# Kernel optimization log

Measured on AMD Instinct MI355X. Metric: run time of the kernel, lower is better.

The kernel has to match this reference:

```python
import jax, jax.numpy as jnp
import numpy as np

DIM = 1024
C = 128
B = 8
T = 2048


def setup_inputs() -> dict:
    key = jax.random.key(0)
    ks = jax.random.split(key, 16)
    s = 0.02
    inp = {
        "x": jax.random.normal(ks[0], (B, T, DIM), dtype=jnp.float32),
        "Wq": jax.random.normal(ks[1], (DIM, C), dtype=jnp.float32) * s,
        "bq": jnp.zeros((C,), dtype=jnp.float32),
        "Wk": jax.random.normal(ks[2], (DIM, C), dtype=jnp.float32) * s,
        "bk": jnp.zeros((C,), dtype=jnp.float32),
        "Wv": jax.random.normal(ks[3], (DIM, C), dtype=jnp.float32) * s,
        "bv": jnp.zeros((C,), dtype=jnp.float32),
        "Wa": jax.random.normal(ks[4], (DIM, 1), dtype=jnp.float32) * s,
        "ba": jnp.zeros((1,), dtype=jnp.float32),
        "Wb": jax.random.normal(ks[5], (DIM, 1), dtype=jnp.float32) * s,
        "bb": jnp.zeros((1,), dtype=jnp.float32),
        "Wg": jax.random.normal(ks[6], (DIM, C), dtype=jnp.float32) * s,
        "bg": jnp.zeros((C,), dtype=jnp.float32),
        "Wo": jax.random.normal(ks[7], (C, DIM), dtype=jnp.float32) * s,
        "bo": jnp.zeros((DIM,), dtype=jnp.float32),
    }
    return inp


def reference(x, Wq, bq, Wk, bk, Wv, bv, Wa, ba, Wb, bb, Wg, bg, Wo, bo):
    # projections
    q = x @ Wq + bq                                   # [B,T,C]
    kr = x @ Wk + bk
    k = kr / jnp.maximum(jnp.linalg.norm(kr, axis=-1, keepdims=True), 1e-12)  # F.normalize
    v = x @ Wv + bv
    alpha = jax.nn.sigmoid(x @ Wa + ba)               # [B,T,1]
    beta = jax.nn.sigmoid(x @ Wb + bb)                # [B,T,1]
    gate = jax.nn.sigmoid(x @ Wg + bg)                # [B,T,C]

    def step(S, inp):
        q_t, k_t, v_t, a_t, b_t, g_t = inp            # [B,C],[B,C],[B,C],[B,1],[B,1],[B,C]
        # S @ (a*(I - b k k^T)) = a*(S - b*(S k) k^T)  (rank-1 form, no CxC bmm)
        Sk = jnp.einsum('bij,bj->bi', S, k_t)         # [B,C]
        a = a_t[:, :, None]                            # [B,1,1]
        b = b_t[:, :, None]
        S_new = a * (S - b * (Sk[:, :, None] * k_t[:, None, :])) \
                + b * (v_t[:, :, None] * k_t[:, None, :])
        o = jnp.einsum('bi,bij->bj', q_t, S_new) * g_t  # [B,C]
        return S_new, o

    seq = (
        jnp.swapaxes(q, 0, 1), jnp.swapaxes(k, 0, 1), jnp.swapaxes(v, 0, 1),
        jnp.swapaxes(alpha, 0, 1), jnp.swapaxes(beta, 0, 1), jnp.swapaxes(gate, 0, 1),
    )
    S0 = jnp.zeros((x.shape[0], C, C), dtype=x.dtype)
    _, outs = jax.lax.scan(step, S0, seq)             # [T,B,C]
    o = jnp.swapaxes(outs, 0, 1)                      # [B,T,C]
    return o @ Wo + bo                                # [B,T,DIM]
```

## Files before the change

kernel.cpp:

```cpp
#include <hip/hip_runtime.h>
#include <hip/hip_fp16.h>
#include <cstdint>

#define MB 8
#define TT 2048
#define DIMK 1024
#define CC 128
#define NG 32
#define MROWS (MB*TT)
#define NPROJ 576
#define YSTR 576

using bf16x8 = __attribute__((__ext_vector_type__(8))) __bf16;
using f32x4v = __attribute__((__ext_vector_type__(4))) float;
using f32x2v = __attribute__((__ext_vector_type__(2))) float;

__device__ __forceinline__ unsigned short f2b(float f) {
    unsigned u = __float_as_uint(f);
    u += 0x7fffu + ((u >> 16) & 1u);
    return (unsigned short)(u >> 16);
}

__global__ __launch_bounds__(256) void cast_x_kernel(
    const float* __restrict__ in, unsigned short* __restrict__ outp)
{
    size_t i = ((size_t)blockIdx.x * 256 + threadIdx.x) * 8;
    float4 a = *(const float4*)(in + i);
    float4 b = *(const float4*)(in + i + 4);
    uint4 r;
    r.x = f2b(a.x) | ((unsigned)f2b(a.y) << 16);
    r.y = f2b(a.z) | ((unsigned)f2b(a.w) << 16);
    r.z = f2b(b.x) | ((unsigned)f2b(b.y) << 16);
    r.w = f2b(b.z) | ((unsigned)f2b(b.w) << 16);
    *(uint4*)(outp + i) = r;
}

__global__ __launch_bounds__(256) void pack_wt(
    const float* __restrict__ Wq, const float* __restrict__ Wk,
    const float* __restrict__ Wv, const float* __restrict__ Wg,
    const float* __restrict__ Wa, const float* __restrict__ Wb,
    unsigned short* __restrict__ WcatT)
{
    int idx = blockIdx.x * 256 + threadIdx.x;
    if (idx >= NPROJ * DIMK) return;
    int n = idx >> 10, k = idx & 1023;
    float v = 0.f;
    if      (n < 128) v = Wq[k * 128 + n];
    else if (n < 256) v = Wk[k * 128 + (n - 128)];
    else if (n < 384) v = Wv[k * 128 + (n - 256)];
    else if (n < 512) v = Wg[k * 128 + (n - 384)];
    else if (n == 512) v = Wa[k];
    else if (n == 513) v = Wb[k];
    WcatT[idx] = f2b(v);
}

__global__ void pack_bias(const float* __restrict__ bq, const float* __restrict__ bk,
                          const float* __restrict__ bv, const float* __restrict__ bg,
                          const float* __restrict__ ba, const float* __restrict__ bb,
                          float* __restrict__ biascat)
{
    int n = threadIdx.x;
    if (n >= NPROJ) return;
    float v = 0.f;
    if      (n < 128) v = bq[n];
    else if (n < 256) v = bk[n - 128];
    else if (n < 384) v = bv[n - 256];
    else if (n < 512) v = bg[n - 384];
    else if (n == 512) v = ba[0];
    else if (n == 513) v = bb[0];
    biascat[n] = v;
}

__global__ __launch_bounds__(256) void cast_wot(
    const float* __restrict__ Wo, unsigned short* __restrict__ WoT)
{
    int idx = blockIdx.x * 256 + threadIdx.x;
    if (idx >= DIMK * CC) return;
    int n = idx >> 7, k = idx & 127;
    WoT[idx] = f2b(Wo[k * DIMK + n]);
}

__global__ __launch_bounds__(256) void gemm_bt_bf16(
    const unsigned short* __restrict__ A, const unsigned short* __restrict__ BT,
    const float* __restrict__ bias, float* __restrict__ C,
    int M, int N, int K)
{
    __shared__ unsigned short As[4][128][8];
    __shared__ unsigned short Bs[4][64][8];
    int tid = threadIdx.x;
    int w = tid >> 6, l = tid & 63;
    int lm = l & 15, lq = l >> 4;
    int bm = blockIdx.y * 128, bn = blockIdx.x * 64;

    f32x4v acc[2][4];
#pragma unroll
    for (int rt = 0; rt < 2; rt++)
#pragma unroll
        for (int ct = 0; ct < 4; ct++) acc[rt][ct] = (f32x4v)(0.f);

    int ar = tid >> 1, ah = tid & 1;
    int brn = tid >> 2, bq = tid & 3;
    const unsigned short* Arow = A + (size_t)(bm + ar) * K + ah * 16;
    const unsigned short* Brow = BT + (size_t)(bn + brn) * K + bq * 8;

    for (int kk = 0; kk < K; kk += 32) {
        uint4 av0 = *(const uint4*)(Arow + kk);
        uint4 av1 = *(const uint4*)(Arow + kk + 8);
        uint4 bv  = *(const uint4*)(Brow + kk);
        __syncthreads();
        *(uint4*)&As[ah * 2][ar][0]     = av0;
        *(uint4*)&As[ah * 2 + 1][ar][0] = av1;
        *(uint4*)&Bs[bq][brn][0]        = bv;
        __syncthreads();
        bf16x8 af[2], bf[4];
#pragma unroll
        for (int rt = 0; rt < 2; rt++)
            __builtin_memcpy(&af[rt], &As[lq][w * 32 + rt * 16 + lm][0], 16);
#pragma unroll
        for (int ct = 0; ct < 4; ct++)
            __builtin_memcpy(&bf[ct], &Bs[lq][ct * 16 + lm][0], 16);
#pragma unroll
        for (int rt = 0; rt < 2; rt++)
#pragma unroll
            for (int ct = 0; ct < 4; ct++)
                acc[rt][ct] = __builtin_amdgcn_mfma_f32_16x16x32_bf16(
                    af[rt], bf[ct], acc[rt][ct], 0, 0, 0);
    }
#pragma unroll
    for (int rt = 0; rt < 2; rt++)
#pragma unroll
        for (int ct = 0; ct < 4; ct++) {
            int col = bn + ct * 16 + lm;
            float bcol = bias[col];
#pragma unroll
            for (int i = 0; i < 4; i++) {
                int row = bm + w * 32 + rt * 16 + lq * 4 + i;
                C[(size_t)row * N + col] = acc[rt][ct][i] + bcol;
            }
        }
}

__global__ __launch_bounds__(64) void postproj_kernel(
    const float* __restrict__ Y, float* __restrict__ knorm,
    float* __restrict__ gbuf, float4* __restrict__ qvab)
{
    int m = blockIdx.x;
    int lane = threadIdx.x;
    int b = m >> 11, t = m & (TT - 1);
    const float* yr = Y + (size_t)m * YSTR;
    float k0 = yr[128 + lane], k1 = yr[192 + lane];
    float ss = k0 * k0 + k1 * k1;
#pragma unroll
    for (int mask = 1; mask < 64; mask <<= 1) ss += __shfl_xor(ss, mask);
    float inv = 1.0f / fmaxf(sqrtf(ss), 1e-12f);
    knorm[(size_t)m * CC + lane]      = k0 * inv;
    knorm[(size_t)m * CC + 64 + lane] = k1 * inv;
    float g0 = yr[384 + lane], g1 = yr[448 + lane];
    gbuf[(size_t)m * CC + lane]      = 1.f / (1.f + expf(-g0));
    gbuf[(size_t)m * CC + 64 + lane] = 1.f / (1.f + expf(-g1));
    float a  = 1.f / (1.f + expf(-yr[512]));
    float bb = 1.f / (1.f + expf(-yr[513]));
    {
        int i = lane;
        qvab[((size_t)(b * NG + (i >> 2)) * TT + t) * 4 + (i & 3)] =
            make_float4(yr[i], yr[256 + i], a, bb);
        i = lane + 64;
        qvab[((size_t)(b * NG + (i >> 2)) * TT + t) * 4 + (i & 3)] =
            make_float4(yr[i], yr[256 + i], a, bb);
    }
}

__device__ __forceinline__ float dpp_add_xor1(float p) {
    int i = __builtin_amdgcn_mov_dpp(__float_as_int(p), 0xB1, 0xF, 0xF, true);
    return p + __int_as_float(i);
}
__device__ __forceinline__ float dpp_add_xor2(float p) {
    int i = __builtin_amdgcn_mov_dpp(__float_as_int(p), 0x4E, 0xF, 0xF, true);
    return p + __int_as_float(i);
}
__device__ __forceinline__ float dpp_add_mirror7(float p) {
    int i = __builtin_amdgcn_mov_dpp(__float_as_int(p), 0x141, 0xF, 0xF, true);
    return p + __int_as_float(i);
}
__device__ __forceinline__ float dpp_add_ror8(float p) {
    int i = __builtin_amdgcn_mov_dpp(__float_as_int(p), 0x128, 0xF, 0xF, true);
    return p + __int_as_float(i);
}
__device__ __forceinline__ int h2i(__half2 h) { int i; __builtin_memcpy(&i, &h, 4); return i; }
__device__ __forceinline__ __half2 i2h(int i) { __half2 h; __builtin_memcpy(&h, &i, 4); return h; }

__device__ __forceinline__ f32x2v vfma2(f32x2v a, f32x2v b, f32x2v c) {
#if __has_builtin(__builtin_elementwise_fma)
    return __builtin_elementwise_fma(a, b, c);
#else
    return a * b + c;
#endif
}
__device__ __forceinline__ __half2 cvt2h(f32x2v v) {
    return __float22half2_rn(make_float2(v.x, v.y));
}

__device__ __forceinline__ void pl16_swap(unsigned &a, unsigned &b) {
#if __has_builtin(__builtin_amdgcn_permlane16_swap)
    auto r = __builtin_amdgcn_permlane16_swap(a, b, false, false);
    a = (unsigned)r[0]; b = (unsigned)r[1];
#else
    asm volatile("v_permlane16_swap_b32 %0, %1" : "+v"(a), "+v"(b));
#endif
}
__device__ __forceinline__ void pl32_swap(unsigned &a, unsigned &b) {
#if __has_builtin(__builtin_amdgcn_permlane32_swap)
    auto r = __builtin_amdgcn_permlane32_swap(a, b, false, false);
    a = (unsigned)r[0]; b = (unsigned)r[1];
#else
    asm volatile("v_permlane32_swap_b32 %0, %1" : "+v"(a), "+v"(b));
#endif
}
__device__ __forceinline__ float pl16_add(float p) {
    unsigned a = __float_as_uint(p), b = a;
    pl16_swap(a, b);
    return __uint_as_float(a) + __uint_as_float(b);
}
__device__ __forceinline__ float pl32_add(float p) {
    unsigned a = __float_as_uint(p), b = a;
    pl32_swap(a, b);
    return __uint_as_float(a) + __uint_as_float(b);
}

__device__ __forceinline__ void gload_lds16(const void* g, void* l) {
    __builtin_amdgcn_global_load_lds(
        (const __attribute__((address_space(1))) void*)g,
        (__attribute__((address_space(3))) void*)l, 16, 0, 0);
}

#define CH  32
#define NCH (TT/CH)

template <bool ATOMIC>
__global__ __launch_bounds__(256, 1) void scan_kernel(
    const float* __restrict__ knorm, const float4* __restrict__ qvab,
    void* __restrict__ outp)
{
    __shared__ float lk[2 * CH * 128];
    __shared__ float lq[2 * CH * 16];
    __shared__ unsigned outb[2 * 4 * CH * 64];

    int blk = blockIdx.x;
    int b = blk >> 5;
    int gi = blk & 31;
    int tid = threadIdx.x;
    int w = tid >> 6, lane = tid & 63;
    f32x2v s2v = (f32x2v)(0.f);
    size_t mbase = (size_t)b * TT;

    const char* kgb = (const char*)(knorm + mbase * CC);
    const char* qgb = (const char*)(qvab + (size_t)blk * TT * 4);
    size_t lane16 = (size_t)lane * 16;

#define STAGE_CHUNK(cc, bf) do {                                              \
    char* lkd = (char*)lk + (size_t)(bf) * (CH * 512) + (size_t)w * 4096;     \
    const char* kc_ = kgb + (size_t)(cc) * (CH * 512) + (size_t)w * 4096;     \
    _Pragma("unroll")                                                         \
    for (int i_ = 0; i_ < 4; ++i_)                                            \
        gload_lds16(kc_ + (size_t)i_ * 1024 + lane16, lkd + i_ * 1024);       \
    if (w == 0) {                                                             \
        char* lqd = (char*)lq + (size_t)(bf) * (CH * 64);                     \
        const char* qc_ = qgb + (size_t)(cc) * (CH * 64);                     \
        gload_lds16(qc_ + lane16, lqd);                                       \
        gload_lds16(qc_ + 1024 + lane16, lqd + 1024);                         \
    }                                                                         \
} while (0)

#define LDK(st, sl) do {                                                      \
    kP[sl] = *(const f32x2v*)(lkc + (st) * 128 + lane * 2);                   \
    qP[sl] = *(const f32x4v*)(lqc + (st) * 16 + w * 4);                       \
} while (0)

#define KSTEP(st, sl) do {                                                    \
    f32x2v k2 = kP[sl];                                                       \
    f32x4v qv = qP[sl];                                                       \
    float q_ = qv[0], v_ = qv[1], at_ = qv[2], bt_ = qv[3];                   \
    f32x2v ps_ = s2v * k2;                                                    \
    float p_ = ps_[0] + ps_[1];                                               \
    p_ = dpp_add_xor1(p_);                                                    \
    p_ = dpp_add_xor2(p_);                                                    \
    p_ = dpp_add_mirror7(p_);                                                 \
    p_ = dpp_add_ror8(p_);                                                    \
    p_ = pl16_add(p_);                                                        \
    p_ = pl32_add(p_);                                                        \
    float ba_ = at_ * bt_, bv_ = bt_ * v_;                                    \
    float cr_ = fmaf(-ba_, p_, bv_);                                          \
    f32x2v at2_ = {at_, at_};                                                 \
    f32x2v cr2_ = {cr_, cr_};                                                 \
    f32x2v q2_  = {q_, q_};                                                   \
    s2v = vfma2(k2, cr2_, s2v * at2_);                                        \
    __half2 pb_ = cvt2h(q2_ * s2v);                                           \
    obw[(st) * 64] = (unsigned)h2i(pb_);                                      \
} while (0)

#define COMBINE(cc) do {                                                      \
    const unsigned* ob_ = outb + (size_t)((cc) & 1) * (4 * CH * 64);          \
    int tg_ = (cc) * CH;                                                      \
    _Pragma("unroll")                                                         \
    for (int j_ = 0; j_ < 8; ++j_) {                                          \
        int slot_ = tid + 256 * j_;                                           \
        int st_ = slot_ >> 6, ln_ = slot_ & 63;                               \
        __half2 h0_ = i2h((int)ob_[(0 * CH + st_) * 64 + ln_]);               \
        __half2 h1_ = i2h((int)ob_[(1 * CH + st_) * 64 + ln_]);               \
        __half2 h2_ = i2h((int)ob_[(2 * CH + st_) * 64 + ln_]);               \
        __half2 h3_ = i2h((int)ob_[(3 * CH + st_) * 64 + ln_]);               \
        __half2 r_ = __hadd2(__hadd2(h0_, h1_), __hadd2(h2_, h3_));           \
        size_t m_ = mbase + tg_ + st_;                                        \
        if (ATOMIC) {                                                         \
            float2 f_ = __half22float2(r_);                                   \
            float* op_ = (float*)outp + m_ * CC + ln_ * 2;                    \
            atomicAdd(op_, f_.x);                                             \
            atomicAdd(op_ + 1, f_.y);                                         \
        } else {                                                              \
            ((unsigned*)outp)[((size_t)gi * MROWS + m_) * 64 + ln_] =         \
                (unsigned)h2i(r_);                                            \
        }                                                                     \
    }                                                                         \
} while (0)

    STAGE_CHUNK(0, 0);

    for (int c = 0; c < NCH; ++c) {
        int cur = c & 1;
        if (c + 1 < NCH) STAGE_CHUNK(c + 1, cur ^ 1);
        if (c < 2) {
            asm volatile("s_waitcnt vmcnt(4)" ::: "memory");
        } else if (c + 1 < NCH) {
            asm volatile("s_waitcnt vmcnt(12)" ::: "memory");
        } else {
            asm volatile("s_waitcnt vmcnt(8)" ::: "memory");
        }
        asm volatile("s_waitcnt lgkmcnt(0)" ::: "memory");
        __builtin_amdgcn_s_barrier();
        if (c > 0) COMBINE(c - 1);

        const float* lkc = lk + (size_t)cur * CH * 128;
        const float* lqc = lq + (size_t)cur * CH * 16;
        unsigned* obw = outb + (size_t)(cur * 4 + w) * CH * 64 + lane;

        f32x2v kP[4];
        f32x4v qP[4];
        LDK(0, 0); LDK(1, 1); LDK(2, 2);
#pragma unroll
        for (int st = 0; st < CH; ++st) {
            if (st + 3 < CH) LDK(st + 3, (st + 3) & 3);
            KSTEP(st, st & 3);
        }
    }
    asm volatile("s_waitcnt lgkmcnt(0)" ::: "memory");
    __builtin_amdgcn_s_barrier();
    COMBINE(NCH - 1);
#undef STAGE_CHUNK
#undef LDK
#undef KSTEP
#undef COMBINE
}

__global__ __launch_bounds__(256) void combine_kernel(
    const unsigned* __restrict__ opart,
    const float* __restrict__ gbuf, unsigned* __restrict__ ocombb)
{
    size_t idx = (size_t)blockIdx.x * 256 + threadIdx.x;
    float sx = 0.f, sy = 0.f;
#pragma unroll
    for (int gi = 0; gi < NG; ++gi) {
        __half2 h = i2h((int)opart[(size_t)gi * MROWS * 64 + idx]);
        float2 f = __half22float2(h);
        sx += f.x; sy += f.y;
    }
    float2 g = *(const float2*)(gbuf + idx * 2);
    ocombb[idx] = f2b(sx * g.x) | ((unsigned)f2b(sy * g.y) << 16);
}

__global__ __launch_bounds__(256) void gate_kernel(
    const float* __restrict__ ocombf, const float* __restrict__ gbuf,
    unsigned short* __restrict__ ocombb)
{
    size_t idx = (size_t)blockIdx.x * 256 + threadIdx.x;
    ocombb[idx] = f2b(ocombf[idx] * gbuf[idx]);
}

extern "C" void kernel_launch(void* const* d_in, const int* in_sizes, int n_in,
                              void* d_out, int out_size, void* d_ws, size_t ws_size,
                              hipStream_t stream)
{
    const float* x  = (const float*)d_in[0];
    const float* Wq = (const float*)d_in[1];
    const float* bq = (const float*)d_in[2];
    const float* Wk = (const float*)d_in[3];
    const float* bk = (const float*)d_in[4];
    const float* Wv = (const float*)d_in[5];
    const float* bv = (const float*)d_in[6];
    const float* Wa = (const float*)d_in[7];
    const float* ba = (const float*)d_in[8];
    const float* Wb = (const float*)d_in[9];
    const float* bb = (const float*)d_in[10];
    const float* Wg = (const float*)d_in[11];
    const float* bg = (const float*)d_in[12];
    const float* Wo = (const float*)d_in[13];
    const float* bo = (const float*)d_in[14];
    float* out = (float*)d_out;

    float* ws = (float*)d_ws;
    size_t off = 0;
    float* knorm   = ws + off; off += (size_t)MROWS * CC;
    float* gbuf    = ws + off; off += (size_t)MROWS * CC;
    unsigned* ocombb = (unsigned*)(ws + off); off += (size_t)MROWS * CC / 2;
    unsigned short* WcatT = (unsigned short*)(ws + off); off += (size_t)NPROJ * DIMK / 2;
    unsigned short* WoT   = (unsigned short*)(ws + off); off += (size_t)DIMK * CC / 2;
    float* biascat = ws + off; off += NPROJ;
    unsigned short* xb = (unsigned short*)(ws + off);
    float* qvab    = ws + off; off += (size_t)MROWS * DIMK / 2;
    float* Y       = ws + off;
    size_t opart_off = off;
    off += (size_t)MROWS * YSTR;
    float* ocombf  = ws + opart_off;
    unsigned* opart = (unsigned*)(ws + opart_off);
    size_t opart_end = opart_off + (size_t)NG * MROWS * 64;
    size_t need_big = (opart_end > off ? opart_end : off) * sizeof(float);
    bool big = ws_size >= need_big;

    hipLaunchKernelGGL(cast_x_kernel, dim3((size_t)MROWS * DIMK / 8 / 256), dim3(256), 0, stream,
                       x, xb);
    hipLaunchKernelGGL(pack_wt, dim3(NPROJ * DIMK / 256), dim3(256), 0, stream,
                       Wq, Wk, Wv, Wg, Wa, Wb, WcatT);
    hipLaunchKernelGGL(pack_bias, dim3(1), dim3(NPROJ), 0, stream,
                       bq, bk, bv, bg, ba, bb, biascat);
    hipLaunchKernelGGL(cast_wot, dim3(DIMK * CC / 256), dim3(256), 0, stream,
                       Wo, WoT);
    hipLaunchKernelGGL(gemm_bt_bf16, dim3(NPROJ / 64, MROWS / 128), dim3(256), 0, stream,
                       xb, WcatT, biascat, Y, MROWS, NPROJ, DIMK);
    hipLaunchKernelGGL(postproj_kernel, dim3(MROWS), dim3(64), 0, stream,
                       Y, knorm, gbuf, (float4*)qvab);
    if (big) {
        hipLaunchKernelGGL((scan_kernel<false>), dim3(MB * NG), dim3(256), 0, stream,
                           knorm, (const float4*)qvab, (void*)opart);
        hipLaunchKernelGGL(combine_kernel, dim3(MROWS * 64 / 256), dim3(256), 0, stream,
                           opart, gbuf, ocombb);
    } else {
        (void)hipMemsetAsync(ocombf, 0, (size_t)MROWS * CC * sizeof(float), stream);
        hipLaunchKernelGGL((scan_kernel<true>), dim3(MB * NG), dim3(256), 0, stream,
                           knorm, (const float4*)qvab, (void*)ocombf);
        hipLaunchKernelGGL(gate_kernel, dim3(MROWS * CC / 256), dim3(256), 0, stream,
                           ocombf, gbuf, (unsigned short*)ocombb);
    }
    hipLaunchKernelGGL(gemm_bt_bf16, dim3(DIMK / 64, MROWS / 128), dim3(256), 0, stream,
                       (const unsigned short*)ocombb, WoT, bo, out, MROWS, DIMK, CC);
}
```

Measured before the change: 440.0 us.

## Software-pipeline scan reduction for next step and interleave combine into step loop

Restructures the sequential scan step so the cross-lane reduction of S·k for the next timestep is computed right after the state update, which shortens the dependency chain at the start of each step. The previous-chunk combine work, which used to run as a single block after the barrier, is split into eight pieces interleaved every four steps so its LDS reads and global writes overlap with the serial recurrence. This adds some register pressure and extra code in the unrolled loop, and the first step of each chunk recomputes the reduction from LDS.

```diff
diff --git a/kernel.cpp b/kernel.cpp
--- a/kernel.cpp
+++ b/kernel.cpp
@@ -226,6 +226,15 @@
     pl32_swap(a, b);
     return __uint_as_float(a) + __uint_as_float(b);
 }
+__device__ __forceinline__ float red6(float h) {
+    h = dpp_add_xor1(h);
+    h = dpp_add_xor2(h);
+    h = dpp_add_mirror7(h);
+    h = dpp_add_ror8(h);
+    h = pl16_add(h);
+    h = pl32_add(h);
+    return h;
+}
 
 __device__ __forceinline__ void gload_lds16(const void* g, void* l) {
     __builtin_amdgcn_global_load_lds(
@@ -251,6 +260,7 @@
     int tid = threadIdx.x;
     int w = tid >> 6, lane = tid & 63;
     f32x2v s2v = (f32x2v)(0.f);
+    float pred = 0.f;
     size_t mbase = (size_t)b * TT;
 
     const char* kgb = (const char*)(knorm + mbase * CC);
@@ -276,50 +286,24 @@
     qP[sl] = *(const f32x4v*)(lqc + (st) * 16 + w * 4);                       \
 } while (0)
 
-#define KSTEP(st, sl) do {                                                    \
-    f32x2v k2 = kP[sl];                                                       \
-    f32x4v qv = qP[sl];                                                       \
-    float q_ = qv[0], v_ = qv[1], at_ = qv[2], bt_ = qv[3];                   \
-    f32x2v ps_ = s2v * k2;                                                    \
-    float p_ = ps_[0] + ps_[1];                                               \
-    p_ = dpp_add_xor1(p_);                                                    \
-    p_ = dpp_add_xor2(p_);                                                    \
-    p_ = dpp_add_mirror7(p_);                                                 \
-    p_ = dpp_add_ror8(p_);                                                    \
-    p_ = pl16_add(p_);                                                        \
-    p_ = pl32_add(p_);                                                        \
-    float ba_ = at_ * bt_, bv_ = bt_ * v_;                                    \
-    float cr_ = fmaf(-ba_, p_, bv_);                                          \
-    f32x2v at2_ = {at_, at_};                                                 \
-    f32x2v cr2_ = {cr_, cr_};                                                 \
-    f32x2v q2_  = {q_, q_};                                                   \
-    s2v = vfma2(k2, cr2_, s2v * at2_);                                        \
-    __half2 pb_ = cvt2h(q2_ * s2v);                                           \
-    obw[(st) * 64] = (unsigned)h2i(pb_);                                      \
-} while (0)
-
-#define COMBINE(cc) do {                                                      \
+#define COMBINE_ONE(cc, j_) do {                                              \
     const unsigned* ob_ = outb + (size_t)((cc) & 1) * (4 * CH * 64);          \
-    int tg_ = (cc) * CH;                                                      \
-    _Pragma("unroll")                                                         \
-    for (int j_ = 0; j_ < 8; ++j_) {                                          \
-        int slot_ = tid + 256 * j_;                                           \
-        int st_ = slot_ >> 6, ln_ = slot_ & 63;                               \
-        __half2 h0_ = i2h((int)ob_[(0 * CH + st_) * 64 + ln_]);               \
-        __half2 h1_ = i2h((int)ob_[(1 * CH + st_) * 64 + ln_]);               \
-        __half2 h2_ = i2h((int)ob_[(2 * CH + st_) * 64 + ln_]);               \
-        __half2 h3_ = i2h((int)ob_[(3 * CH + st_) * 64 + ln_]);               \
-        __half2 r_ = __hadd2(__hadd2(h0_, h1_), __hadd2(h2_, h3_));           \
-        size_t m_ = mbase + tg_ + st_;                                        \
-        if (ATOMIC) {                                                         \
-            float2 f_ = __half22float2(r_);                                   \
-            float* op_ = (float*)outp + m_ * CC + ln_ * 2;                    \
-            atomicAdd(op_, f_.x);                                             \
-            atomicAdd(op_ + 1, f_.y);                                         \
-        } else {                                                              \
-            ((unsigned*)outp)[((size_t)gi * MROWS + m_) * 64 + ln_] =         \
-                (unsigned)h2i(r_);                                            \
-        }                                                                     \
+    int slot_ = tid + 256 * (j_);                                             \
+    int st_ = slot_ >> 6, ln_ = slot_ & 63;                                   \
+    __half2 h0_ = i2h((int)ob_[(0 * CH + st_) * 64 + ln_]);                   \
+    __half2 h1_ = i2h((int)ob_[(1 * CH + st_) * 64 + ln_]);                   \
+    __half2 h2_ = i2h((int)ob_[(2 * CH + st_) * 64 + ln_]);                   \
+    __half2 h3_ = i2h((int)ob_[(3 * CH + st_) * 64 + ln_]);                   \
+    __half2 r_ = __hadd2(__hadd2(h0_, h1_), __hadd2(h2_, h3_));               \
+    size_t m_ = mbase + (size_t)(cc) * CH + st_;                              \
+    if (ATOMIC) {                                                             \
+        float2 f_ = __half22float2(r_);                                       \
+        float* op_ = (float*)outp + m_ * CC + ln_ * 2;                        \
+        atomicAdd(op_, f_.x);                                                 \
+        atomicAdd(op_ + 1, f_.y);                                             \
+    } else {                                                                  \
+        ((unsigned*)outp)[((size_t)gi * MROWS + m_) * 64 + ln_] =             \
+            (unsigned)h2i(r_);                                                \
     }                                                                         \
 } while (0)
 
@@ -337,28 +321,49 @@
         }
         asm volatile("s_waitcnt lgkmcnt(0)" ::: "memory");
         __builtin_amdgcn_s_barrier();
-        if (c > 0) COMBINE(c - 1);
 
         const float* lkc = lk + (size_t)cur * CH * 128;
         const float* lqc = lq + (size_t)cur * CH * 16;
         unsigned* obw = outb + (size_t)(cur * 4 + w) * CH * 64 + lane;
 
+        if (c > 0) {
+            f32x2v kb = *(const f32x2v*)(lkc + lane * 2);
+            f32x2v nb = s2v * kb;
+            pred = red6(nb[0] + nb[1]);
+        }
+
         f32x2v kP[4];
         f32x4v qP[4];
         LDK(0, 0); LDK(1, 1); LDK(2, 2);
 #pragma unroll
         for (int st = 0; st < CH; ++st) {
             if (st + 3 < CH) LDK(st + 3, (st + 3) & 3);
-            KSTEP(st, st & 3);
+            f32x2v k2 = kP[st & 3];
+            f32x4v qv = qP[st & 3];
+            float q_ = qv[0], v_ = qv[1], at_ = qv[2], bt_ = qv[3];
+            float ba_ = at_ * bt_, bv_ = bt_ * v_;
+            float cr_ = fmaf(-ba_, pred, bv_);
+            f32x2v at2_ = {at_, at_};
+            f32x2v cr2_ = {cr_, cr_};
+            f32x2v q2_  = {q_, q_};
+            s2v = vfma2(k2, cr2_, s2v * at2_);
+            __half2 pb_ = cvt2h(q2_ * s2v);
+            obw[st * 64] = (unsigned)h2i(pb_);
+            if (st < CH - 1) {
+                f32x2v kn = kP[(st + 1) & 3];
+                f32x2v ns = s2v * kn;
+                pred = red6(ns[0] + ns[1]);
+            }
+            if ((st & 3) == 3 && c > 0) COMBINE_ONE(c - 1, st >> 2);
         }
     }
     asm volatile("s_waitcnt lgkmcnt(0)" ::: "memory");
     __builtin_amdgcn_s_barrier();
-    COMBINE(NCH - 1);
+#pragma unroll
+    for (int j = 0; j < 8; ++j) COMBINE_ONE(NCH - 1, j);
 #undef STAGE_CHUNK
 #undef LDK
-#undef KSTEP
-#undef COMBINE
+#undef COMBINE_ONE
 }
 
 __global__ __launch_bounds__(256) void combine_kernel(
```

Measured after the change: 465.4 us. +5.8%, slower.

## Double-buffer GEMM tiles with direct global-to-LDS async loads

Applied to the files above, without the earlier changes.

The bf16 projection GEMM now loads its A and B tiles with global_load_lds directly into shared memory, instead of going through registers. Shared memory is double-buffered so the next k-step's loads are in flight while MFMAs run on the current buffer, with explicit vmcnt waits and barriers. The aim is to hide global memory latency and cut register staging in the GEMM. It doubles LDS use and relies on hand-placed waitcnt and barriers being correct.

```diff
diff --git a/kernel.cpp b/kernel.cpp
--- a/kernel.cpp
+++ b/kernel.cpp
@@ -19,6 +19,12 @@
     unsigned u = __float_as_uint(f);
     u += 0x7fffu + ((u >> 16) & 1u);
     return (unsigned short)(u >> 16);
+}
+
+__device__ __forceinline__ void gload_lds16(const void* g, void* l) {
+    __builtin_amdgcn_global_load_lds(
+        (const __attribute__((address_space(1))) void*)g,
+        (__attribute__((address_space(3))) void*)l, 16, 0, 0);
 }
 
 __global__ __launch_bounds__(256) void cast_x_kernel(
@@ -85,8 +91,8 @@
     const float* __restrict__ bias, float* __restrict__ C,
     int M, int N, int K)
 {
-    __shared__ unsigned short As[4][128][8];
-    __shared__ unsigned short Bs[4][64][8];
+    __shared__ unsigned short As[2][4][128][8];
+    __shared__ unsigned short Bs[2][4][64][8];
     int tid = threadIdx.x;
     int w = tid >> 6, l = tid & 63;
     int lm = l & 15, lq = l >> 4;
@@ -98,34 +104,43 @@
 #pragma unroll
         for (int ct = 0; ct < 4; ct++) acc[rt][ct] = (f32x4v)(0.f);
 
-    int ar = tid >> 1, ah = tid & 1;
-    int brn = tid >> 2, bq = tid & 3;
-    const unsigned short* Arow = A + (size_t)(bm + ar) * K + ah * 16;
-    const unsigned short* Brow = BT + (size_t)(bn + brn) * K + bq * 8;
-
-    for (int kk = 0; kk < K; kk += 32) {
-        uint4 av0 = *(const uint4*)(Arow + kk);
-        uint4 av1 = *(const uint4*)(Arow + kk + 8);
-        uint4 bv  = *(const uint4*)(Brow + kk);
-        __syncthreads();
-        *(uint4*)&As[ah * 2][ar][0]     = av0;
-        *(uint4*)&As[ah * 2 + 1][ar][0] = av1;
-        *(uint4*)&Bs[bq][brn][0]        = bv;
-        __syncthreads();
+    const char* Asrc0 = (const char*)(A + (size_t)(bm + l) * K) + w * 16;
+    const char* Asrc1 = (const char*)(A + (size_t)(bm + 64 + l) * K) + w * 16;
+    const char* Bsrc  = (const char*)(BT + (size_t)(bn + l) * K) + w * 16;
+
+#define GSTAGE(kk, bf) do {                                                   \
+    gload_lds16(Asrc0 + (size_t)(kk) * 2, &As[bf][w][0][0]);                  \
+    gload_lds16(Asrc1 + (size_t)(kk) * 2, &As[bf][w][64][0]);                 \
+    gload_lds16(Bsrc  + (size_t)(kk) * 2, &Bs[bf][w][0][0]);                  \
+} while (0)
+
+    GSTAGE(0, 0);
+    int nk = K >> 5;
+    for (int ik = 0; ik < nk; ++ik) {
+        int bufc = ik & 1;
+        if (ik + 1 < nk) {
+            GSTAGE((ik + 1) << 5, bufc ^ 1);
+            asm volatile("s_waitcnt vmcnt(3)" ::: "memory");
+        } else {
+            asm volatile("s_waitcnt vmcnt(0)" ::: "memory");
+        }
+        __builtin_amdgcn_s_barrier();
         bf16x8 af[2], bf[4];
 #pragma unroll
         for (int rt = 0; rt < 2; rt++)
-            __builtin_memcpy(&af[rt], &As[lq][w * 32 + rt * 16 + lm][0], 16);
+            __builtin_memcpy(&af[rt], &As[bufc][lq][w * 32 + rt * 16 + lm][0], 16);
 #pragma unroll
         for (int ct = 0; ct < 4; ct++)
-            __builtin_memcpy(&bf[ct], &Bs[lq][ct * 16 + lm][0], 16);
+            __builtin_memcpy(&bf[ct], &Bs[bufc][lq][ct * 16 + lm][0], 16);
 #pragma unroll
         for (int rt = 0; rt < 2; rt++)
 #pragma unroll
             for (int ct = 0; ct < 4; ct++)
                 acc[rt][ct] = __builtin_amdgcn_mfma_f32_16x16x32_bf16(
                     af[rt], bf[ct], acc[rt][ct], 0, 0, 0);
+        __builtin_amdgcn_s_barrier();
     }
+#undef GSTAGE
 #pragma unroll
     for (int rt = 0; rt < 2; rt++)
 #pragma unroll
@@ -225,12 +240,6 @@
     unsigned a = __float_as_uint(p), b = a;
     pl32_swap(a, b);
     return __uint_as_float(a) + __uint_as_float(b);
-}
-
-__device__ __forceinline__ void gload_lds16(const void* g, void* l) {
-    __builtin_amdgcn_global_load_lds(
-        (const __attribute__((address_space(1))) void*)g,
-        (__attribute__((address_space(3))) void*)l, 16, 0, 0);
 }
 
 #define CH  32
```

New measurement: 465.2 us. +5.7%, slower.

## Process two state rows per wave in scan kernel with 128-thread blocks

Applied to the files above, without the earlier changes.

The scan kernel now runs with 2 waves per block instead of 4, and each wave carries two independent state rows (sA, sB) whose reductions and updates are interleaved. Staging, output buffering, the combine loop and the waitcnt thresholds are adjusted to the halved thread count. The aim is to hide the latency of the serial DPP/permlane reduction chain by giving each wave two independent dependency chains, and to cut per-block wave count. In exchange each wave does twice the work per step and issues more LDS loads, so per-step latency could grow if the interleaving does not fill the gaps.

```diff
diff --git a/kernel.cpp b/kernel.cpp
--- a/kernel.cpp
+++ b/kernel.cpp
@@ -19,6 +19,12 @@
     unsigned u = __float_as_uint(f);
     u += 0x7fffu + ((u >> 16) & 1u);
     return (unsigned short)(u >> 16);
+}
+
+__device__ __forceinline__ void gload_lds16(const void* g, void* l) {
+    __builtin_amdgcn_global_load_lds(
+        (const __attribute__((address_space(1))) void*)g,
+        (__attribute__((address_space(3))) void*)l, 16, 0, 0);
 }
 
 __global__ __launch_bounds__(256) void cast_x_kernel(
@@ -227,17 +233,11 @@
     return __uint_as_float(a) + __uint_as_float(b);
 }
 
-__device__ __forceinline__ void gload_lds16(const void* g, void* l) {
-    __builtin_amdgcn_global_load_lds(
-        (const __attribute__((address_space(1))) void*)g,
-        (__attribute__((address_space(3))) void*)l, 16, 0, 0);
-}
-
 #define CH  32
 #define NCH (TT/CH)
 
 template <bool ATOMIC>
-__global__ __launch_bounds__(256, 1) void scan_kernel(
+__global__ __launch_bounds__(128, 1) void scan_kernel(
     const float* __restrict__ knorm, const float4* __restrict__ qvab,
     void* __restrict__ outp)
 {
@@ -250,7 +250,9 @@
     int gi = blk & 31;
     int tid = threadIdx.x;
     int w = tid >> 6, lane = tid & 63;
-    f32x2v s2v = (f32x2v)(0.f);
+    int ra = 2 * w, rb = 2 * w + 1;
+    f32x2v sA = (f32x2v)(0.f);
+    f32x2v sB = (f32x2v)(0.f);
     size_t mbase = (size_t)b * TT;
 
     const char* kgb = (const char*)(knorm + mbase * CC);
@@ -258,52 +260,58 @@
     size_t lane16 = (size_t)lane * 16;
 
 #define STAGE_CHUNK(cc, bf) do {                                              \
-    char* lkd = (char*)lk + (size_t)(bf) * (CH * 512) + (size_t)w * 4096;     \
-    const char* kc_ = kgb + (size_t)(cc) * (CH * 512) + (size_t)w * 4096;     \
+    char* lkd = (char*)lk + (size_t)(bf) * (CH * 512) + (size_t)w * 8192;     \
+    const char* kc_ = kgb + (size_t)(cc) * (CH * 512) + (size_t)w * 8192;     \
     _Pragma("unroll")                                                         \
-    for (int i_ = 0; i_ < 4; ++i_)                                            \
+    for (int i_ = 0; i_ < 8; ++i_)                                            \
         gload_lds16(kc_ + (size_t)i_ * 1024 + lane16, lkd + i_ * 1024);       \
-    if (w == 0) {                                                             \
-        char* lqd = (char*)lq + (size_t)(bf) * (CH * 64);                     \
-        const char* qc_ = qgb + (size_t)(cc) * (CH * 64);                     \
+    {                                                                         \
+        char* lqd = (char*)lq + (size_t)(bf) * (CH * 64) + (size_t)w * 1024;  \
+        const char* qc_ = qgb + (size_t)(cc) * (CH * 64) + (size_t)w * 1024;  \
         gload_lds16(qc_ + lane16, lqd);                                       \
-        gload_lds16(qc_ + 1024 + lane16, lqd + 1024);                         \
     }                                                                         \
 } while (0)
 
 #define LDK(st, sl) do {                                                      \
     kP[sl] = *(const f32x2v*)(lkc + (st) * 128 + lane * 2);                   \
-    qP[sl] = *(const f32x4v*)(lqc + (st) * 16 + w * 4);                       \
+    qPa[sl] = *(const f32x4v*)(lqc + (st) * 16 + ra * 4);                     \
+    qPb[sl] = *(const f32x4v*)(lqc + (st) * 16 + rb * 4);                     \
 } while (0)
 
-#define KSTEP(st, sl) do {                                                    \
+#define KSTEP2(st, sl) do {                                                   \
     f32x2v k2 = kP[sl];                                                       \
-    f32x4v qv = qP[sl];                                                       \
-    float q_ = qv[0], v_ = qv[1], at_ = qv[2], bt_ = qv[3];                   \
-    f32x2v ps_ = s2v * k2;                                                    \
-    float p_ = ps_[0] + ps_[1];                                               \
-    p_ = dpp_add_xor1(p_);                                                    \
-    p_ = dpp_add_xor2(p_);                                                    \
-    p_ = dpp_add_mirror7(p_);                                                 \
-    p_ = dpp_add_ror8(p_);                                                    \
-    p_ = pl16_add(p_);                                                        \
-    p_ = pl32_add(p_);                                                        \
-    float ba_ = at_ * bt_, bv_ = bt_ * v_;                                    \
-    float cr_ = fmaf(-ba_, p_, bv_);                                          \
-    f32x2v at2_ = {at_, at_};                                                 \
-    f32x2v cr2_ = {cr_, cr_};                                                 \
-    f32x2v q2_  = {q_, q_};                                                   \
-    s2v = vfma2(k2, cr2_, s2v * at2_);                                        \
-    __half2 pb_ = cvt2h(q2_ * s2v);                                           \
-    obw[(st) * 64] = (unsigned)h2i(pb_);                                      \
+    f32x4v qa = qPa[sl];                                                      \
+    f32x4v qb = qPb[sl];                                                      \
+    f32x2v psa = sA * k2;                                                     \
+    f32x2v psb = sB * k2;                                                     \
+    float pa = psa[0] + psa[1];                                               \
+    float pb = psb[0] + psb[1];                                               \
+    pa = dpp_add_xor1(pa);    pb = dpp_add_xor1(pb);                          \
+    pa = dpp_add_xor2(pa);    pb = dpp_add_xor2(pb);                          \
+    pa = dpp_add_mirror7(pa); pb = dpp_add_mirror7(pb);                       \
+    pa = dpp_add_ror8(pa);    pb = dpp_add_ror8(pb);                          \
+    pa = pl16_add(pa);        pb = pl16_add(pb);                              \
+    pa = pl32_add(pa);        pb = pl32_add(pb);                              \
+    float baA = qa[2] * qa[3], bvA = qa[3] * qa[1];                           \
+    float baB = qb[2] * qb[3], bvB = qb[3] * qb[1];                           \
+    float crA = fmaf(-baA, pa, bvA);                                          \
+    float crB = fmaf(-baB, pb, bvB);                                          \
+    f32x2v atA = {qa[2], qa[2]}, crA2 = {crA, crA}, q2A = {qa[0], qa[0]};     \
+    f32x2v atB = {qb[2], qb[2]}, crB2 = {crB, crB}, q2B = {qb[0], qb[0]};     \
+    sA = vfma2(k2, crA2, sA * atA);                                           \
+    sB = vfma2(k2, crB2, sB * atB);                                           \
+    __half2 pbA = cvt2h(q2A * sA);                                            \
+    __half2 pbB = cvt2h(q2B * sB);                                            \
+    obwA[(st) * 64] = (unsigned)h2i(pbA);                                     \
+    obwB[(st) * 64] = (unsigned)h2i(pbB);                                     \
 } while (0)
 
 #define COMBINE(cc) do {                                                      \
     const unsigned* ob_ = outb + (size_t)((cc) & 1) * (4 * CH * 64);          \
     int tg_ = (cc) * CH;                                                      \
     _Pragma("unroll")                                                         \
-    for (int j_ = 0; j_ < 8; ++j_) {                                          \
-        int slot_ = tid + 256 * j_;                                           \
+    for (int j_ = 0; j_ < 16; ++j_) {                                         \
+        int slot_ = tid + 128 * j_;                                           \
         int st_ = slot_ >> 6, ln_ = slot_ & 63;                               \
         __half2 h0_ = i2h((int)ob_[(0 * CH + st_) * 64 + ln_]);               \
         __half2 h1_ = i2h((int)ob_[(1 * CH + st_) * 64 + ln_]);               \
@@ -329,11 +337,11 @@
         int cur = c & 1;
         if (c + 1 < NCH) STAGE_CHUNK(c + 1, cur ^ 1);
         if (c < 2) {
-            asm volatile("s_waitcnt vmcnt(4)" ::: "memory");
+            asm volatile("s_waitcnt vmcnt(9)" ::: "memory");
         } else if (c + 1 < NCH) {
-            asm volatile("s_waitcnt vmcnt(12)" ::: "memory");
+            asm volatile("s_waitcnt vmcnt(25)" ::: "memory");
         } else {
-            asm volatile("s_waitcnt vmcnt(8)" ::: "memory");
+            asm volatile("s_waitcnt vmcnt(16)" ::: "memory");
         }
         asm volatile("s_waitcnt lgkmcnt(0)" ::: "memory");
         __builtin_amdgcn_s_barrier();
@@ -341,15 +349,16 @@
 
         const float* lkc = lk + (size_t)cur * CH * 128;
         const float* lqc = lq + (size_t)cur * CH * 16;
-        unsigned* obw = outb + (size_t)(cur * 4 + w) * CH * 64 + lane;
+        unsigned* obwA = outb + (size_t)(cur * 4 + ra) * CH * 64 + lane;
+        unsigned* obwB = outb + (size_t)(cur * 4 + rb) * CH * 64 + lane;
 
         f32x2v kP[4];
-        f32x4v qP[4];
+        f32x4v qPa[4], qPb[4];
         LDK(0, 0); LDK(1, 1); LDK(2, 2);
 #pragma unroll
         for (int st = 0; st < CH; ++st) {
             if (st + 3 < CH) LDK(st + 3, (st + 3) & 3);
-            KSTEP(st, st & 3);
+            KSTEP2(st, st & 3);
         }
     }
     asm volatile("s_waitcnt lgkmcnt(0)" ::: "memory");
@@ -357,7 +366,7 @@
     COMBINE(NCH - 1);
 #undef STAGE_CHUNK
 #undef LDK
-#undef KSTEP
+#undef KSTEP2
 #undef COMBINE
 }
 
@@ -438,13 +447,13 @@
     hipLaunchKernelGGL(postproj_kernel, dim3(MROWS), dim3(64), 0, stream,
                        Y, knorm, gbuf, (float4*)qvab);
     if (big) {
-        hipLaunchKernelGGL((scan_kernel<false>), dim3(MB * NG), dim3(256), 0, stream,
+        hipLaunchKernelGGL((scan_kernel<false>), dim3(MB * NG), dim3(128), 0, stream,
                            knorm, (const float4*)qvab, (void*)opart);
         hipLaunchKernelGGL(combine_kernel, dim3(MROWS * 64 / 256), dim3(256), 0, stream,
                            opart, gbuf, ocombb);
     } else {
         (void)hipMemsetAsync(ocombf, 0, (size_t)MROWS * CC * sizeof(float), stream);
-        hipLaunchKernelGGL((scan_kernel<true>), dim3(MB * NG), dim3(256), 0, stream,
+        hipLaunchKernelGGL((scan_kernel<true>), dim3(MB * NG), dim3(128), 0, stream,
                            knorm, (const float4*)qvab, (void*)ocombf);
         hipLaunchKernelGGL(gate_kernel, dim3(MROWS * CC / 256), dim3(256), 0, stream,
                            ocombf, gbuf, (unsigned short*)ocombb);
```

After: 541.6 us. 1.23x slower.
